# Kernel optimization log

Hardware: AMD Instinct MI355X
Metric: run time of the kernel (lower is better)

Reference implementation:

```python
import jax, jax.numpy as jnp
import numpy as np

N_NODES = 50000
N_EDGES = 800000
IN_DIM = 16
H1, H2, H3, HFC = 64, 128, 256, 256


def setup_inputs() -> dict:
    key = jax.random.key(0)
    ks = jax.random.split(key, 8)
    w = lambda k, s: jax.random.normal(k, s, dtype=jnp.float32) * 0.05
    return {
        "X": jax.random.normal(ks[0], (N_NODES, IN_DIM), dtype=jnp.float32),
        "edge_index": jax.random.randint(ks[1], (2, N_EDGES), 0, N_NODES, dtype=jnp.int64),
        "W1": w(ks[2], (2 * IN_DIM, H1)), "b1": jnp.zeros((H1,), jnp.float32),
        "W2": w(ks[3], (2 * H1, H2)), "b2": jnp.zeros((H2,), jnp.float32),
        "W3": w(ks[4], (2 * H2, H3)), "b3": jnp.zeros((H3,), jnp.float32),
        "Wf1": w(ks[5], (H3, HFC)), "bf1": jnp.zeros((HFC,), jnp.float32),
        "Wf2": w(ks[6], (HFC, 1)), "bf2": jnp.zeros((1,), jnp.float32),
    }


def edge_conv(x, edge_index, W, b):
    # EdgeConv (DGCNN): msg = ReLU(Linear([x_i, x_j - x_i])), max-aggregate at i
    src, dst = edge_index[0], edge_index[1]
    xi = x[dst]                      # [E, d] target node feats
    xj = x[src]                      # [E, d] source node feats
    msg = jax.nn.relu(jnp.concatenate([xi, xj - xi], axis=-1) @ W + b)  # [E, out]
    agg = jax.ops.segment_max(msg, dst, num_segments=x.shape[0])        # [N, out]
    # nodes with no incoming edge get -inf from segment_max -> zero them
    return jnp.where(jnp.isneginf(agg), 0.0, agg)


def reference(X, edge_index, W1, b1, W2, b2, W3, b3, Wf1, bf1, Wf2, bf2):
    H = edge_conv(X, edge_index, W1, b1)
    H = edge_conv(H, edge_index, W2, b2)
    H = edge_conv(H, edge_index, W3, b3)
    # MLP head (dropout is identity at inference)
    H = jax.nn.relu(H @ Wf1 + bf1)
    out = jax.nn.sigmoid(H @ Wf2 + bf2)
    return out.squeeze(-1)  # [N]
```

## Files before the change

### kernel.cpp

```cpp
#include <hip/hip_runtime.h>
#include <math.h>

#define NN 50000
#define NE 800000

typedef unsigned short ushort_t;
typedef __attribute__((ext_vector_type(8))) short bf16x8;
typedef __attribute__((ext_vector_type(4))) float f32x4;

__device__ inline unsigned short f2bf(float f) {
    unsigned int u = __float_as_uint(f);
    u = (u + 0x7fffu + ((u >> 16) & 1u)) >> 16;
    return (unsigned short)u;
}
__device__ inline unsigned int pack2bf(float lo, float hi) {
    return (unsigned int)f2bf(lo) | ((unsigned int)f2bf(hi) << 16);
}

__global__ void zeroi_kernel(int* __restrict__ p, int n) {
    int i = blockIdx.x * blockDim.x + threadIdx.x;
    int s = gridDim.x * blockDim.x;
    for (; i < n; i += s) p[i] = 0;
}

__global__ void hist_kernel(const int* __restrict__ edst, int istride,
                            int* __restrict__ deg, int nE) {
    int i = blockIdx.x * blockDim.x + threadIdx.x;
    int s = gridDim.x * blockDim.x;
    for (; i < nE; i += s) atomicAdd(&deg[edst[(size_t)i * istride]], 1);
}

__global__ __launch_bounds__(256)
void scan_reduce(const int* __restrict__ deg, int* __restrict__ bsum, int n) {
    __shared__ int s[256];
    const int t = threadIdx.x;
    const int i = blockIdx.x * 256 + t;
    s[t] = (i < n) ? deg[i] : 0;
    __syncthreads();
#pragma unroll
    for (int off = 128; off > 0; off >>= 1) {
        if (t < off) s[t] += s[t + off];
        __syncthreads();
    }
    if (t == 0) bsum[blockIdx.x] = s[0];
}

__global__ __launch_bounds__(256)
void scan_tops(const int* __restrict__ bsum, int* __restrict__ boff,
               int* __restrict__ rowptr, int nb, int n) {
    __shared__ int s[256];
    const int t = threadIdx.x;
    const int v = (t < nb) ? bsum[t] : 0;
    s[t] = v;
    __syncthreads();
    for (int off = 1; off < 256; off <<= 1) {
        int u = (t >= off) ? s[t - off] : 0;
        __syncthreads();
        s[t] += u;
        __syncthreads();
    }
    if (t < nb) boff[t] = s[t] - v;
    if (t == 255) rowptr[n] = s[255];
}

__global__ __launch_bounds__(256)
void scan_apply(int* __restrict__ deg, const int* __restrict__ boff,
                int* __restrict__ rowptr, int n) {
    __shared__ int s[256];
    const int t = threadIdx.x;
    const int i = blockIdx.x * 256 + t;
    const int v = (i < n) ? deg[i] : 0;
    s[t] = v;
    __syncthreads();
    for (int off = 1; off < 256; off <<= 1) {
        int u = (t >= off) ? s[t - off] : 0;
        __syncthreads();
        s[t] += u;
        __syncthreads();
    }
    if (i < n) {
        int ex = boff[blockIdx.x] + s[t] - v;
        rowptr[i] = ex;
        deg[i] = ex;
    }
}

__global__ void scatter_kernel(const int* __restrict__ esrc, const int* __restrict__ edst,
                               int istride, int* __restrict__ cursor,
                               int* __restrict__ col, int nE) {
    int i = blockIdx.x * blockDim.x + threadIdx.x;
    int s = gridDim.x * blockDim.x;
    for (; i < nE; i += s) {
        int d = edst[(size_t)i * istride];
        int pos = atomicAdd(&cursor[d], 1);
        col[pos] = esrc[(size_t)i * istride];
    }
}

__global__ void prepwt1_kernel(const float* __restrict__ W, ushort_t* __restrict__ Wt) {
    int idx = blockIdx.x * blockDim.x + threadIdx.x;
    if (idx >= 128 * 32) return;
    int o = idx / 32, k = idx % 32;
    float v = 0.f;
    if (k < 16)
        v = (o < 64) ? (W[k * 64 + o] - W[(k + 16) * 64 + o])
                     : W[(k + 16) * 64 + (o - 64)];
    Wt[idx] = f2bf(v);
}

__global__ void xpad_kernel(const float* __restrict__ X, ushort_t* __restrict__ Xb, int n) {
    int idx = blockIdx.x * blockDim.x + threadIdx.x;
    int s = gridDim.x * blockDim.x;
    for (; idx < n * 32; idx += s) {
        int row = idx >> 5, c = idx & 31;
        Xb[idx] = (c < 16) ? f2bf(X[(size_t)row * 16 + c]) : (ushort_t)0;
    }
}

__global__ void prepwt_kernel(const float* __restrict__ W, ushort_t* __restrict__ Wt,
                              int IN, int OUT) {
    int idx = blockIdx.x * blockDim.x + threadIdx.x;
    if (idx >= 2 * OUT * IN) return;
    int o = idx / IN, k = idx % IN;
    float v = (o < OUT) ? (W[(size_t)k * OUT + o] - W[(size_t)(k + IN) * OUT + o])
                        : W[(size_t)(k + IN) * OUT + (o - OUT)];
    Wt[idx] = f2bf(v);
}

__global__ void transw_kernel(const float* __restrict__ W, ushort_t* __restrict__ Wt,
                              int K, int N) {
    int idx = blockIdx.x * blockDim.x + threadIdx.x;
    if (idx >= K * N) return;
    int nn = idx / K, k = idx % K;
    Wt[idx] = f2bf(W[(size_t)k * N + nn]);
}

template<int K, int OUT, int NF, int MR>
__global__ __launch_bounds__(256)
void gemm_mfma(const ushort_t* __restrict__ A, const ushort_t* __restrict__ Wt,
               float* __restrict__ P, ushort_t* __restrict__ Qb, int n) {
    constexpr int KB = K / 32;
    const int wave = threadIdx.x >> 6;
    const int lane = threadIdx.x & 63;
    const int lr = lane & 15;
    const int kg = lane >> 4;
    const int row0 = (blockIdx.x * 4 + wave) * (MR * 16);
    const int col0 = blockIdx.y * (NF * 16);

    f32x4 acc[MR][NF];
#pragma unroll
    for (int m = 0; m < MR; ++m)
#pragma unroll
        for (int f = 0; f < NF; ++f) acc[m][f] = (f32x4)(0.f);

    const ushort_t* Ap[MR];
#pragma unroll
    for (int m = 0; m < MR; ++m) {
        int arow = row0 + m * 16 + lr;
        if (arow >= n) arow = n - 1;
        Ap[m] = A + (size_t)arow * K + kg * 8;
    }
    const ushort_t* Bp = Wt + (size_t)(col0 + lr) * K + kg * 8;

#pragma unroll
    for (int kb = 0; kb < KB; ++kb) {
        bf16x8 af[MR];
#pragma unroll
        for (int m = 0; m < MR; ++m) af[m] = *(const bf16x8*)(Ap[m] + kb * 32);
        bf16x8 bfv[NF];
#pragma unroll
        for (int f = 0; f < NF; ++f)
            bfv[f] = *(const bf16x8*)(Bp + (size_t)f * 16 * K + kb * 32);
#pragma unroll
        for (int f = 0; f < NF; ++f)
#pragma unroll
            for (int m = 0; m < MR; ++m)
                acc[m][f] = __builtin_amdgcn_mfma_f32_16x16x32_bf16(af[m], bfv[f], acc[m][f], 0, 0, 0);
    }

#pragma unroll
    for (int m = 0; m < MR; ++m) {
#pragma unroll
        for (int f = 0; f < NF; ++f) {
#pragma unroll
            for (int r = 0; r < 4; ++r) {
                int row = row0 + m * 16 + kg * 4 + r;
                if (row < n) {
                    int c = col0 + f * 16 + lr;
                    float v = acc[m][f][r];
                    if (c < OUT) P[(size_t)row * OUT + c] = v;
                    else Qb[(size_t)row * OUT + (c - OUT)] = f2bf(v);
                }
            }
        }
    }
}

__global__ __launch_bounds__(256)
void head_mfma(const ushort_t* __restrict__ H, const ushort_t* __restrict__ Wf1t,
               const float* __restrict__ bf1, const float* __restrict__ Wf2,
               float* __restrict__ hacc, int n) {
    const int wave = threadIdx.x >> 6;
    const int lane = threadIdx.x & 63;
    const int row0 = (blockIdx.x * 4 + wave) * 16;
    const int col0 = blockIdx.y * 128;
    const int lr = lane & 15;
    const int kg = lane >> 4;

    f32x4 acc[8];
#pragma unroll
    for (int i = 0; i < 8; ++i) acc[i] = (f32x4)(0.f);

    int arow = row0 + lr;
    if (arow >= n) arow = n - 1;
    const ushort_t* Aptr = H + (size_t)arow * 256 + kg * 8;
    const ushort_t* Bp = Wf1t + (size_t)(col0 + lr) * 256 + kg * 8;

#pragma unroll
    for (int kb = 0; kb < 8; ++kb) {
        bf16x8 afrag = *(const bf16x8*)(Aptr + kb * 32);
        bf16x8 bfv[8];
#pragma unroll
        for (int nf = 0; nf < 8; ++nf)
            bfv[nf] = *(const bf16x8*)(Bp + (size_t)nf * 16 * 256 + kb * 32);
#pragma unroll
        for (int nf = 0; nf < 8; ++nf)
            acc[nf] = __builtin_amdgcn_mfma_f32_16x16x32_bf16(afrag, bfv[nf], acc[nf], 0, 0, 0);
    }

    float part[4] = {0.f, 0.f, 0.f, 0.f};
#pragma unroll
    for (int nf = 0; nf < 8; ++nf) {
        int c = col0 + nf * 16 + lr;
        float w2 = Wf2[c];
        float bb = bf1[c];
#pragma unroll
        for (int r = 0; r < 4; ++r)
            part[r] = fmaf(fmaxf(acc[nf][r] + bb, 0.f), w2, part[r]);
    }
#pragma unroll
    for (int s = 1; s < 16; s <<= 1) {
#pragma unroll
        for (int r = 0; r < 4; ++r) part[r] += __shfl_xor(part[r], s, 16);
    }
    if (lr == 0) {
#pragma unroll
        for (int r = 0; r < 4; ++r) {
            int row = row0 + kg * 4 + r;
            if (row < n) atomicAdd(&hacc[row], part[r]);
        }
    }
}

__global__ void zerof_kernel(float* __restrict__ p, int n) {
    int i = blockIdx.x * blockDim.x + threadIdx.x;
    int s = gridDim.x * blockDim.x;
    for (; i < n; i += s) p[i] = 0.f;
}

__global__ void sigmoid_kernel(const float* __restrict__ hacc, const float* __restrict__ bf2,
                               float* __restrict__ out, int n) {
    int i = blockIdx.x * blockDim.x + threadIdx.x;
    int s = gridDim.x * blockDim.x;
    float b = bf2[0];
    for (; i < n; i += s) out[i] = 1.f / (1.f + expf(-(hacc[i] + b)));
}

template<int OUT>
__global__ __launch_bounds__(256, 8)
void segmax_combine(const float* __restrict__ P, const ushort_t* __restrict__ Qb,
                    const int* __restrict__ rowptr, const int* __restrict__ col,
                    const float* __restrict__ bias, ushort_t* __restrict__ Hout, int n) {
    constexpr int G = OUT / 8;
    constexpr int NPB = 256 / G;
    const int gid = threadIdx.x / G;
    const int lane = threadIdx.x % G;
    const int i = blockIdx.x * NPB + gid;
    if (i >= n) return;

    const int r0 = rowptr[i];
    const int r1 = rowptr[i + 1];
    const int c8 = lane * 8;

    float m[8];
#pragma unroll
    for (int j = 0; j < 8; ++j) m[j] = -INFINITY;

    auto domax = [&](uint4 q) {
        m[0] = fmaxf(m[0], __uint_as_float(q.x << 16));
        m[1] = fmaxf(m[1], __uint_as_float(q.x & 0xffff0000u));
        m[2] = fmaxf(m[2], __uint_as_float(q.y << 16));
        m[3] = fmaxf(m[3], __uint_as_float(q.y & 0xffff0000u));
        m[4] = fmaxf(m[4], __uint_as_float(q.z << 16));
        m[5] = fmaxf(m[5], __uint_as_float(q.z & 0xffff0000u));
        m[6] = fmaxf(m[6], __uint_as_float(q.w << 16));
        m[7] = fmaxf(m[7], __uint_as_float(q.w & 0xffff0000u));
    };

    int r = r0;
    for (; r + 1 < r1; r += 2) {
        int s0 = col[r];
        int s1 = col[r + 1];
        uint4 qa = *(const uint4*)(Qb + (size_t)s0 * OUT + c8);
        uint4 qb = *(const uint4*)(Qb + (size_t)s1 * OUT + c8);
        domax(qa);
        domax(qb);
    }
    if (r < r1) {
        int s0 = col[r];
        domax(*(const uint4*)(Qb + (size_t)s0 * OUT + c8));
    }

    const float4 p0 = *(const float4*)(P + (size_t)i * OUT + c8);
    const float4 p1 = *(const float4*)(P + (size_t)i * OUT + c8 + 4);
    const float4 b0 = *(const float4*)(bias + c8);
    const float4 b1 = *(const float4*)(bias + c8 + 4);

    float h[8];
    h[0] = fmaxf(p0.x + b0.x + m[0], 0.f);
    h[1] = fmaxf(p0.y + b0.y + m[1], 0.f);
    h[2] = fmaxf(p0.z + b0.z + m[2], 0.f);
    h[3] = fmaxf(p0.w + b0.w + m[3], 0.f);
    h[4] = fmaxf(p1.x + b1.x + m[4], 0.f);
    h[5] = fmaxf(p1.y + b1.y + m[5], 0.f);
    h[6] = fmaxf(p1.z + b1.z + m[6], 0.f);
    h[7] = fmaxf(p1.w + b1.w + m[7], 0.f);

    uint4 o;
    o.x = pack2bf(h[0], h[1]);
    o.y = pack2bf(h[2], h[3]);
    o.z = pack2bf(h[4], h[5]);
    o.w = pack2bf(h[6], h[7]);
    *(uint4*)(Hout + (size_t)i * OUT + c8) = o;
}

extern "C" void kernel_launch(void* const* d_in, const int* in_sizes, int n_in,
                              void* d_out, int out_size, void* d_ws, size_t ws_size,
                              hipStream_t stream) {
    const float* X   = (const float*)d_in[0];
    const int*   ei  = (const int*)d_in[1];
    const float* W1  = (const float*)d_in[2];
    const float* b1  = (const float*)d_in[3];
    const float* W2  = (const float*)d_in[4];
    const float* b2  = (const float*)d_in[5];
    const float* W3  = (const float*)d_in[6];
    const float* b3  = (const float*)d_in[7];
    const float* Wf1 = (const float*)d_in[8];
    const float* bf1 = (const float*)d_in[9];
    const float* Wf2 = (const float*)d_in[10];
    const float* bf2 = (const float*)d_in[11];
    float* out = (float*)d_out;

    int istride = (in_sizes[1] == 4 * NE) ? 2 : 1;
    const int* esrc = ei;
    const int* edst = ei + (size_t)NE * istride;

    float*    P      = (float*)d_ws;
    ushort_t* Qb     = (ushort_t*)(P + (size_t)NN * 256);
    ushort_t* Ha     = Qb + (size_t)NN * 256;
    ushort_t* Hb     = Ha + (size_t)NN * 256;
    int*      rowptr = (int*)(Hb + (size_t)NN * 256);
    int*      deg    = rowptr + (NN + 8);
    int*      col    = deg + NN;
    int*      bsum   = col + NE;
    int*      boff   = bsum + 256;
    ushort_t* Wt1    = (ushort_t*)(boff + 256);
    ushort_t* Wt2    = Wt1 + 128 * 32;
    ushort_t* Wt3    = Wt2 + 256 * 64;
    ushort_t* Wf1t   = Wt3 + 512 * 128;
    ushort_t* Xb     = Wf1t + 256 * 256;
    float*    hacc   = (float*)(Xb + (size_t)NN * 32);

    const int NB = (NN + 255) / 256;

    zeroi_kernel<<<256, 256, 0, stream>>>(deg, NN);
    hist_kernel<<<1024, 256, 0, stream>>>(edst, istride, deg, NE);
    scan_reduce<<<NB, 256, 0, stream>>>(deg, bsum, NN);
    scan_tops<<<1, 256, 0, stream>>>(bsum, boff, rowptr, NB, NN);
    scan_apply<<<NB, 256, 0, stream>>>(deg, boff, rowptr, NN);
    scatter_kernel<<<1024, 256, 0, stream>>>(esrc, edst, istride, deg, col, NE);

    prepwt1_kernel<<<(128 * 32 + 255) / 256, 256, 0, stream>>>(W1, Wt1);
    prepwt_kernel<<<(2 * 128 * 64 + 255) / 256, 256, 0, stream>>>(W2, Wt2, 64, 128);
    prepwt_kernel<<<(2 * 256 * 128 + 255) / 256, 256, 0, stream>>>(W3, Wt3, 128, 256);
    transw_kernel<<<(256 * 256 + 255) / 256, 256, 0, stream>>>(Wf1, Wf1t, 256, 256);
    xpad_kernel<<<1024, 256, 0, stream>>>(X, Xb, NN);

    const int GB = (NN + 127) / 128;

    {
        dim3 g(GB, 1);
        gemm_mfma<32, 64, 8, 2><<<g, 256, 0, stream>>>(Xb, Wt1, P, Qb, NN);
    }
    segmax_combine<64><<<(NN * 8 + 255) / 256, 256, 0, stream>>>(P, Qb, rowptr, col, b1, Ha, NN);

    {
        dim3 g(GB, 2);
        gemm_mfma<64, 128, 8, 2><<<g, 256, 0, stream>>>(Ha, Wt2, P, Qb, NN);
    }
    segmax_combine<128><<<(NN * 16 + 255) / 256, 256, 0, stream>>>(P, Qb, rowptr, col, b2, Hb, NN);

    {
        dim3 g(GB, 4);
        gemm_mfma<128, 256, 8, 2><<<g, 256, 0, stream>>>(Hb, Wt3, P, Qb, NN);
    }
    segmax_combine<256><<<(NN * 32 + 255) / 256, 256, 0, stream>>>(P, Qb, rowptr, col, b3, Ha, NN);

    zerof_kernel<<<64, 256, 0, stream>>>(hacc, NN);
    {
        dim3 g((NN + 63) / 64, 2);
        head_mfma<<<g, 256, 0, stream>>>(Ha, Wf1t, bf1, Wf2, hacc, NN);
    }
    sigmoid_kernel<<<64, 256, 0, stream>>>(hacc, bf2, out, NN);
}
```

Baseline: 367.7 us.

## Merge prep kernels, store P in bf16 interleaved with Q, fold bias into GEMM

Several small setup kernels (weight transposes, X padding, hacc zeroing, deg zeroing) are merged into two kernels to cut launch count. The edge indices are first compacted into int32 arrays, so hist and scatter read contiguous data. The GEMM now adds the bias and writes P and Q together as one bf16 row-interleaved buffer, which halves P traffic and drops the bias loads in segmax. The segmax gather loop is unrolled by four. Rounding P to bf16 loses some precision, and the interleaved layout doubles the row stride of the Q gathers.

```diff
diff --git a/kernel.cpp b/kernel.cpp
--- a/kernel.cpp
+++ b/kernel.cpp
@@ -17,17 +17,24 @@
     return (unsigned int)f2bf(lo) | ((unsigned int)f2bf(hi) << 16);
 }
 
-__global__ void zeroi_kernel(int* __restrict__ p, int n) {
+__global__ void prep0_kernel(const int* __restrict__ ei, int istride,
+                             int* __restrict__ esrc32, int* __restrict__ edst32,
+                             int* __restrict__ deg) {
     int i = blockIdx.x * blockDim.x + threadIdx.x;
     int s = gridDim.x * blockDim.x;
-    for (; i < n; i += s) p[i] = 0;
-}
-
-__global__ void hist_kernel(const int* __restrict__ edst, int istride,
-                            int* __restrict__ deg, int nE) {
+    for (int j = i; j < NN; j += s) deg[j] = 0;
+    const int* eis = ei;
+    const int* eid = ei + (size_t)NE * istride;
+    for (int j = i; j < NE; j += s) {
+        esrc32[j] = eis[(size_t)j * istride];
+        edst32[j] = eid[(size_t)j * istride];
+    }
+}
+
+__global__ void hist_kernel(const int* __restrict__ edst, int* __restrict__ deg, int nE) {
     int i = blockIdx.x * blockDim.x + threadIdx.x;
     int s = gridDim.x * blockDim.x;
-    for (; i < nE; i += s) atomicAdd(&deg[edst[(size_t)i * istride]], 1);
+    for (; i < nE; i += s) atomicAdd(&deg[edst[i]], 1);
 }
 
 __global__ __launch_bounds__(256)
@@ -86,59 +93,65 @@
 }
 
 __global__ void scatter_kernel(const int* __restrict__ esrc, const int* __restrict__ edst,
-                               int istride, int* __restrict__ cursor,
-                               int* __restrict__ col, int nE) {
+                               int* __restrict__ cursor, int* __restrict__ col, int nE) {
     int i = blockIdx.x * blockDim.x + threadIdx.x;
     int s = gridDim.x * blockDim.x;
     for (; i < nE; i += s) {
-        int d = edst[(size_t)i * istride];
+        int d = edst[i];
         int pos = atomicAdd(&cursor[d], 1);
-        col[pos] = esrc[(size_t)i * istride];
-    }
-}
-
-__global__ void prepwt1_kernel(const float* __restrict__ W, ushort_t* __restrict__ Wt) {
-    int idx = blockIdx.x * blockDim.x + threadIdx.x;
-    if (idx >= 128 * 32) return;
-    int o = idx / 32, k = idx % 32;
-    float v = 0.f;
-    if (k < 16)
-        v = (o < 64) ? (W[k * 64 + o] - W[(k + 16) * 64 + o])
-                     : W[(k + 16) * 64 + (o - 64)];
-    Wt[idx] = f2bf(v);
-}
-
-__global__ void xpad_kernel(const float* __restrict__ X, ushort_t* __restrict__ Xb, int n) {
-    int idx = blockIdx.x * blockDim.x + threadIdx.x;
+        col[pos] = esrc[i];
+    }
+}
+
+__global__ void megaprep_kernel(const float* __restrict__ W1, const float* __restrict__ W2,
+                                const float* __restrict__ W3, const float* __restrict__ Wf1,
+                                const float* __restrict__ X,
+                                ushort_t* __restrict__ Wt1, ushort_t* __restrict__ Wt2,
+                                ushort_t* __restrict__ Wt3, ushort_t* __restrict__ Wf1t,
+                                ushort_t* __restrict__ Xb, float* __restrict__ hacc) {
+    const int T0 = 128 * 32;
+    const int T1 = T0 + 256 * 64;
+    const int T2 = T1 + 512 * 128;
+    const int T3 = T2 + 256 * 256;
+    const int T4 = T3 + NN * 32;
+    const int T5 = T4 + NN;
+    int i = blockIdx.x * blockDim.x + threadIdx.x;
     int s = gridDim.x * blockDim.x;
-    for (; idx < n * 32; idx += s) {
-        int row = idx >> 5, c = idx & 31;
-        Xb[idx] = (c < 16) ? f2bf(X[(size_t)row * 16 + c]) : (ushort_t)0;
-    }
-}
-
-__global__ void prepwt_kernel(const float* __restrict__ W, ushort_t* __restrict__ Wt,
-                              int IN, int OUT) {
-    int idx = blockIdx.x * blockDim.x + threadIdx.x;
-    if (idx >= 2 * OUT * IN) return;
-    int o = idx / IN, k = idx % IN;
-    float v = (o < OUT) ? (W[(size_t)k * OUT + o] - W[(size_t)(k + IN) * OUT + o])
-                        : W[(size_t)(k + IN) * OUT + (o - OUT)];
-    Wt[idx] = f2bf(v);
-}
-
-__global__ void transw_kernel(const float* __restrict__ W, ushort_t* __restrict__ Wt,
-                              int K, int N) {
-    int idx = blockIdx.x * blockDim.x + threadIdx.x;
-    if (idx >= K * N) return;
-    int nn = idx / K, k = idx % K;
-    Wt[idx] = f2bf(W[(size_t)k * N + nn]);
+    for (; i < T5; i += s) {
+        if (i < T0) {
+            int idx = i, o = idx / 32, k = idx % 32;
+            float v = 0.f;
+            if (k < 16)
+                v = (o < 64) ? (W1[k * 64 + o] - W1[(k + 16) * 64 + o])
+                             : W1[(k + 16) * 64 + (o - 64)];
+            Wt1[idx] = f2bf(v);
+        } else if (i < T1) {
+            int idx = i - T0, o = idx / 64, k = idx % 64;
+            float v = (o < 128) ? (W2[k * 128 + o] - W2[(k + 64) * 128 + o])
+                                : W2[(k + 64) * 128 + (o - 128)];
+            Wt2[idx] = f2bf(v);
+        } else if (i < T2) {
+            int idx = i - T1, o = idx / 128, k = idx % 128;
+            float v = (o < 256) ? (W3[(size_t)k * 256 + o] - W3[(size_t)(k + 128) * 256 + o])
+                                : W3[(size_t)(k + 128) * 256 + (o - 256)];
+            Wt3[idx] = f2bf(v);
+        } else if (i < T3) {
+            int idx = i - T2, nn = idx / 256, k = idx % 256;
+            Wf1t[idx] = f2bf(Wf1[(size_t)k * 256 + nn]);
+        } else if (i < T4) {
+            int idx = i - T3, row = idx >> 5, c = idx & 31;
+            Xb[idx] = (c < 16) ? f2bf(X[(size_t)row * 16 + c]) : (ushort_t)0;
+        } else {
+            hacc[i - T4] = 0.f;
+        }
+    }
 }
 
 template<int K, int OUT, int NF, int MR>
 __global__ __launch_bounds__(256)
 void gemm_mfma(const ushort_t* __restrict__ A, const ushort_t* __restrict__ Wt,
-               float* __restrict__ P, ushort_t* __restrict__ Qb, int n) {
+               const float* __restrict__ bias, ushort_t* __restrict__ PQ, int n) {
+    constexpr int NOUT = 2 * OUT;
     constexpr int KB = K / 32;
     const int wave = threadIdx.x >> 6;
     const int lane = threadIdx.x & 63;
@@ -182,15 +195,12 @@
     for (int m = 0; m < MR; ++m) {
 #pragma unroll
         for (int f = 0; f < NF; ++f) {
+            int c = col0 + f * 16 + lr;
+            float bb = (c < OUT) ? bias[c] : 0.f;
 #pragma unroll
             for (int r = 0; r < 4; ++r) {
                 int row = row0 + m * 16 + kg * 4 + r;
-                if (row < n) {
-                    int c = col0 + f * 16 + lr;
-                    float v = acc[m][f][r];
-                    if (c < OUT) P[(size_t)row * OUT + c] = v;
-                    else Qb[(size_t)row * OUT + (c - OUT)] = f2bf(v);
-                }
+                if (row < n) PQ[(size_t)row * NOUT + c] = f2bf(acc[m][f][r] + bb);
             }
         }
     }
@@ -252,12 +262,6 @@
     }
 }
 
-__global__ void zerof_kernel(float* __restrict__ p, int n) {
-    int i = blockIdx.x * blockDim.x + threadIdx.x;
-    int s = gridDim.x * blockDim.x;
-    for (; i < n; i += s) p[i] = 0.f;
-}
-
 __global__ void sigmoid_kernel(const float* __restrict__ hacc, const float* __restrict__ bf2,
                                float* __restrict__ out, int n) {
     int i = blockIdx.x * blockDim.x + threadIdx.x;
@@ -268,9 +272,9 @@
 
 template<int OUT>
 __global__ __launch_bounds__(256, 8)
-void segmax_combine(const float* __restrict__ P, const ushort_t* __restrict__ Qb,
-                    const int* __restrict__ rowptr, const int* __restrict__ col,
-                    const float* __restrict__ bias, ushort_t* __restrict__ Hout, int n) {
+void segmax_combine(const ushort_t* __restrict__ PQ, const int* __restrict__ rowptr,
+                    const int* __restrict__ col, ushort_t* __restrict__ Hout, int n) {
+    constexpr int NOUT = 2 * OUT;
     constexpr int G = OUT / 8;
     constexpr int NPB = 256 / G;
     const int gid = threadIdx.x / G;
@@ -298,33 +302,28 @@
     };
 
     int r = r0;
-    for (; r + 1 < r1; r += 2) {
-        int s0 = col[r];
-        int s1 = col[r + 1];
-        uint4 qa = *(const uint4*)(Qb + (size_t)s0 * OUT + c8);
-        uint4 qb = *(const uint4*)(Qb + (size_t)s1 * OUT + c8);
-        domax(qa);
-        domax(qb);
-    }
-    if (r < r1) {
-        int s0 = col[r];
-        domax(*(const uint4*)(Qb + (size_t)s0 * OUT + c8));
-    }
-
-    const float4 p0 = *(const float4*)(P + (size_t)i * OUT + c8);
-    const float4 p1 = *(const float4*)(P + (size_t)i * OUT + c8 + 4);
-    const float4 b0 = *(const float4*)(bias + c8);
-    const float4 b1 = *(const float4*)(bias + c8 + 4);
+    for (; r + 3 < r1; r += 4) {
+        int s0 = col[r], s1 = col[r + 1], s2 = col[r + 2], s3 = col[r + 3];
+        uint4 q0 = *(const uint4*)(PQ + (size_t)s0 * NOUT + OUT + c8);
+        uint4 q1 = *(const uint4*)(PQ + (size_t)s1 * NOUT + OUT + c8);
+        uint4 q2 = *(const uint4*)(PQ + (size_t)s2 * NOUT + OUT + c8);
+        uint4 q3 = *(const uint4*)(PQ + (size_t)s3 * NOUT + OUT + c8);
+        domax(q0); domax(q1); domax(q2); domax(q3);
+    }
+    for (; r < r1; ++r) {
+        domax(*(const uint4*)(PQ + (size_t)col[r] * NOUT + OUT + c8));
+    }
+
+    const uint4 pb = *(const uint4*)(PQ + (size_t)i * NOUT + c8);
+    float p[8];
+    p[0] = __uint_as_float(pb.x << 16); p[1] = __uint_as_float(pb.x & 0xffff0000u);
+    p[2] = __uint_as_float(pb.y << 16); p[3] = __uint_as_float(pb.y & 0xffff0000u);
+    p[4] = __uint_as_float(pb.z << 16); p[5] = __uint_as_float(pb.z & 0xffff0000u);
+    p[6] = __uint_as_float(pb.w << 16); p[7] = __uint_as_float(pb.w & 0xffff0000u);
 
     float h[8];
-    h[0] = fmaxf(p0.x + b0.x + m[0], 0.f);
-    h[1] = fmaxf(p0.y + b0.y + m[1], 0.f);
-    h[2] = fmaxf(p0.z + b0.z + m[2], 0.f);
-    h[3] = fmaxf(p0.w + b0.w + m[3], 0.f);
-    h[4] = fmaxf(p1.x + b1.x + m[4], 0.f);
-    h[5] = fmaxf(p1.y + b1.y + m[5], 0.f);
-    h[6] = fmaxf(p1.z + b1.z + m[6], 0.f);
-    h[7] = fmaxf(p1.w + b1.w + m[7], 0.f);
+#pragma unroll
+    for (int j = 0; j < 8; ++j) h[j] = fmaxf(p[j] + m[j], 0.f);
 
     uint4 o;
     o.x = pack2bf(h[0], h[1]);
@@ -352,17 +351,16 @@
     float* out = (float*)d_out;
 
     int istride = (in_sizes[1] == 4 * NE) ? 2 : 1;
-    const int* esrc = ei;
-    const int* edst = ei + (size_t)NE * istride;
-
-    float*    P      = (float*)d_ws;
-    ushort_t* Qb     = (ushort_t*)(P + (size_t)NN * 256);
-    ushort_t* Ha     = Qb + (size_t)NN * 256;
+
+    ushort_t* PQ     = (ushort_t*)d_ws;
+    ushort_t* Ha     = PQ + (size_t)NN * 512;
     ushort_t* Hb     = Ha + (size_t)NN * 256;
     int*      rowptr = (int*)(Hb + (size_t)NN * 256);
     int*      deg    = rowptr + (NN + 8);
     int*      col    = deg + NN;
-    int*      bsum   = col + NE;
+    int*      esrc32 = col + NE;
+    int*      edst32 = esrc32 + NE;
+    int*      bsum   = edst32 + NE;
     int*      boff   = bsum + 256;
     ushort_t* Wt1    = (ushort_t*)(boff + 256);
     ushort_t* Wt2    = Wt1 + 128 * 32;
@@ -373,40 +371,36 @@
 
     const int NB = (NN + 255) / 256;
 
-    zeroi_kernel<<<256, 256, 0, stream>>>(deg, NN);
-    hist_kernel<<<1024, 256, 0, stream>>>(edst, istride, deg, NE);
+    prep0_kernel<<<1024, 256, 0, stream>>>(ei, istride, esrc32, edst32, deg);
+    hist_kernel<<<1024, 256, 0, stream>>>(edst32, deg, NE);
     scan_reduce<<<NB, 256, 0, stream>>>(deg, bsum, NN);
     scan_tops<<<1, 256, 0, stream>>>(bsum, boff, rowptr, NB, NN);
     scan_apply<<<NB, 256, 0, stream>>>(deg, boff, rowptr, NN);
-    scatter_kernel<<<1024, 256, 0, stream>>>(esrc, edst, istride, deg, col, NE);
-
-    prepwt1_kernel<<<(128 * 32 + 255) / 256, 256, 0, stream>>>(W1, Wt1);
-    prepwt_kernel<<<(2 * 128 * 64 + 255) / 256, 256, 0, stream>>>(W2, Wt2, 64, 128);
-    prepwt_kernel<<<(2 * 256 * 128 + 255) / 256, 256, 0, stream>>>(W3, Wt3, 128, 256);
-    transw_kernel<<<(256 * 256 + 255) / 256, 256, 0, stream>>>(Wf1, Wf1t, 256, 256);
-    xpad_kernel<<<1024, 256, 0, stream>>>(X, Xb, NN);
+    scatter_kernel<<<1024, 256, 0, stream>>>(esrc32, edst32, deg, col, NE);
+
+    megaprep_kernel<<<1024, 256, 0, stream>>>(W1, W2, W3, Wf1, X,
+                                              Wt1, Wt2, Wt3, Wf1t, Xb, hacc);
 
     const int GB = (NN + 127) / 128;
 
     {
         dim3 g(GB, 1);
-        gemm_mfma<32, 64, 8, 2><<<g, 256, 0, stream>>>(Xb, Wt1, P, Qb, NN);
-    }
-    segmax_combine<64><<<(NN * 8 + 255) / 256, 256, 0, stream>>>(P, Qb, rowptr, col, b1, Ha, NN);
+        gemm_mfma<32, 64, 8, 2><<<g, 256, 0, stream>>>(Xb, Wt1, b1, PQ, NN);
+    }
+    segmax_combine<64><<<(NN + 31) / 32, 256, 0, stream>>>(PQ, rowptr, col, Ha, NN);
 
     {
         dim3 g(GB, 2);
-        gemm_mfma<64, 128, 8, 2><<<g, 256, 0, stream>>>(Ha, Wt2, P, Qb, NN);
-    }
-    segmax_combine<128><<<(NN * 16 + 255) / 256, 256, 0, stream>>>(P, Qb, rowptr, col, b2, Hb, NN);
+        gemm_mfma<64, 128, 8, 2><<<g, 256, 0, stream>>>(Ha, Wt2, b2, PQ, NN);
+    }
+    segmax_combine<128><<<(NN + 15) / 16, 256, 0, stream>>>(PQ, rowptr, col, Hb, NN);
 
     {
         dim3 g(GB, 4);
-        gemm_mfma<128, 256, 8, 2><<<g, 256, 0, stream>>>(Hb, Wt3, P, Qb, NN);
-    }
-    segmax_combine<256><<<(NN * 32 + 255) / 256, 256, 0, stream>>>(P, Qb, rowptr, col, b3, Ha, NN);
-
-    zerof_kernel<<<64, 256, 0, stream>>>(hacc, NN);
+        gemm_mfma<128, 256, 8, 2><<<g, 256, 0, stream>>>(Hb, Wt3, b3, PQ, NN);
+    }
+    segmax_combine<256><<<(NN + 7) / 8, 256, 0, stream>>>(PQ, rowptr, col, Ha, NN);
+
     {
         dim3 g((NN + 63) / 64, 2);
         head_mfma<<<g, 256, 0, stream>>>(Ha, Wf1t, bf1, Wf2, hacc, NN);
```

After: 377.0 us. +2.5%, slower.
